# Kernel tuning notes

Measured on AMD Instinct MI355X. Metric: run time of the kernel, lower is better.

## Reference

```python
import jax, jax.numpy as jnp
import numpy as np

PAD = 0  # padding_idx from NlpContext

def setup_inputs() -> dict:
    key = jax.random.key(0)
    k1, k2, k3 = jax.random.split(key, 3)
    B, S, O = 64, 2048, 256
    pred = jax.random.normal(k1, (B, S, O), dtype=jnp.float32)
    gt = jax.random.randint(k2, (B, S), 0, O, dtype=jnp.int64)
    transition = jax.random.normal(k3, (O, O), dtype=jnp.float32)
    return {"pred": pred, "gt": gt, "transition": transition}

def reference(pred, gt, transition):
    B, S, O = pred.shape
    mask = (gt == PAD)
    maskf = mask.astype(pred.dtype)  # (B,S)
    # zero padded positions then log_softmax over labels
    pred = pred * (1.0 - maskf[:, :, None])
    logp = jax.nn.log_softmax(pred, axis=-1)          # (B,S,O)
    trans = jax.nn.log_softmax(transition, axis=-1)   # (O,O)

    # --- hypotheses (path) score ---
    # additive recurrence collapses: alpha = logp[:,0] + sum_t rowsum(logp[:,t]) + T*colsum(trans)
    npl = S - jnp.max(jnp.sum(mask.astype(jnp.int32), axis=1))  # non_pad_length
    tvec = jnp.arange(1, S)
    cond = (npl >= 1) & (npl <= S - 1)  # early-break reachable?
    incl = jnp.where(cond, tvec <= npl, True).astype(pred.dtype)  # (S-1,)
    T = incl.sum()
    row_tot = jnp.sum(logp[:, 1:, :], axis=-1)  # (B,S-1)
    alpha = (logp[:, 0, :]
             + jnp.einsum('bt,t->b', row_tot, incl)[:, None]
             + T * jnp.sum(trans, axis=0)[None, :])  # (B,O)

    # --- gold (null hypothesis) score ---
    emit = jnp.take_along_axis(logp, gt[:, :, None], axis=2)[..., 0]  # (B,S)
    tr_sc = trans[gt[:, :-1], gt[:, 1:]] * (1.0 - maskf[:, 1:])       # (B,S-1)
    gold = jnp.sum(tr_sc + emit[:, 1:] + emit[:, 0:1], axis=1)        # (B,)

    return jnp.mean(alpha - gold[:, None])
```

## Files before the change

### kernel.cpp

```cpp
#include <hip/hip_runtime.h>
#include <math.h>

#define Bn 64
#define Sn 2048
#define On 256
#define PAD 0


__launch_bounds__(256)
__global__ void prep_kernel(const float* __restrict__ trans,
                            const int* __restrict__ gt,
                            float* __restrict__ lse_trans,
                            float* __restrict__ row_total,
                            int* __restrict__ padcnt,
                            double* __restrict__ zreg) {
    int blk = blockIdx.x;
    int tid = threadIdx.x, lane = tid & 63, w = tid >> 6;
    if (blk < On) {
        float x = trans[blk * On + tid];
        float se = __expf(x), sx = x;
        #pragma unroll
        for (int off = 32; off > 0; off >>= 1) {
            se += __shfl_xor(se, off);
            sx += __shfl_xor(sx, off);
        }
        __shared__ float s_se[4], s_sx[4];
        if (lane == 0) { s_se[w] = se; s_sx[w] = sx; }
        __syncthreads();
        if (tid == 0) {
            float SE = (s_se[0] + s_se[1]) + (s_se[2] + s_se[3]);
            float SX = (s_sx[0] + s_sx[1]) + (s_sx[2] + s_sx[3]);
            float lse = __logf(SE);
            lse_trans[blk] = lse;
            row_total[blk] = SX - (float)On * lse;
        }
    } else if (blk < On + Bn) {
        int b = blk - On;
        int cnt = 0;
        for (int i = tid; i < Sn; i += 256) cnt += (gt[b * Sn + i] == PAD) ? 1 : 0;
        #pragma unroll
        for (int off = 32; off > 0; off >>= 1) cnt += __shfl_xor(cnt, off);
        __shared__ int s_c[4];
        if (lane == 0) s_c[w] = cnt;
        __syncthreads();
        if (tid == 0) padcnt[b] = (s_c[0] + s_c[1]) + (s_c[2] + s_c[3]);
    } else {
        int idx = (blk - (On + Bn)) * 256 + tid;
        if (idx < 3072) zreg[idx] = 0.0;
    }
}

__launch_bounds__(256)
__global__ void main_kernel(const float* __restrict__ pred,
                            const int* __restrict__ gt,
                            const float* __restrict__ trans,
                            const float* __restrict__ lse_trans,
                            double* __restrict__ bucket,
                            double* __restrict__ accum) {
    int wave = threadIdx.x >> 6, lane = threadIdx.x & 63;
    int base = blockIdx.x * 16 + wave * 4;
    int b = base >> 11;

    const float4* p4 = reinterpret_cast<const float4*>(pred + (size_t)base * On);
    float4 x0 = p4[lane];
    float4 x1 = p4[64 + lane];
    float4 x2 = p4[128 + lane];
    float4 x3 = p4[192 + lane];

    int li = (lane < 5) ? lane : 4;
    int gi = base - 1 + li; if (gi < 0) gi = 0;
    int gv = gt[gi];
    int g0 = __shfl(gv, 1), g1 = __shfl(gv, 2), g2 = __shfl(gv, 3), g3 = __shfl(gv, 4);
    int q0 = __shfl(gv, 0), q1 = g0, q2 = g1, q3 = g2;

    if (g0 == PAD) { x0.x = 0.f; x0.y = 0.f; x0.z = 0.f; x0.w = 0.f; }
    if (g1 == PAD) { x1.x = 0.f; x1.y = 0.f; x1.z = 0.f; x1.w = 0.f; }
    if (g2 == PAD) { x2.x = 0.f; x2.y = 0.f; x2.z = 0.f; x2.w = 0.f; }
    if (g3 == PAD) { x3.x = 0.f; x3.y = 0.f; x3.z = 0.f; x3.w = 0.f; }

    float se0 = (__expf(x0.x) + __expf(x0.y)) + (__expf(x0.z) + __expf(x0.w));
    float se1 = (__expf(x1.x) + __expf(x1.y)) + (__expf(x1.z) + __expf(x1.w));
    float se2 = (__expf(x2.x) + __expf(x2.y)) + (__expf(x2.z) + __expf(x2.w));
    float se3 = (__expf(x3.x) + __expf(x3.y)) + (__expf(x3.z) + __expf(x3.w));
    float sx0 = (x0.x + x0.y) + (x0.z + x0.w);
    float sx1 = (x1.x + x1.y) + (x1.z + x1.w);
    float sx2 = (x2.x + x2.y) + (x2.z + x2.w);
    float sx3 = (x3.x + x3.y) + (x3.z + x3.w);

    #pragma unroll
    for (int off = 32; off > 0; off >>= 1) {
        se0 += __shfl_xor(se0, off); sx0 += __shfl_xor(sx0, off);
        se1 += __shfl_xor(se1, off); sx1 += __shfl_xor(sx1, off);
        se2 += __shfl_xor(se2, off); sx2 += __shfl_xor(sx2, off);
        se3 += __shfl_xor(se3, off); sx3 += __shfl_xor(sx3, off);
    }
    float lse0 = __logf(se0), lse1 = __logf(se1), lse2 = __logf(se2), lse3 = __logf(se3);
    float rs0 = sx0 - (float)On * lse0;
    float rs1 = sx1 - (float)On * lse1;
    float rs2 = sx2 - (float)On * lse2;
    float rs3 = sx3 - (float)On * lse3;

    int c0 = g0 & 3, c1 = g1 & 3, c2 = g2 & 3, c3 = g3 & 3;
    float xv0 = (c0 == 0) ? x0.x : (c0 == 1) ? x0.y : (c0 == 2) ? x0.z : x0.w;
    float xv1 = (c1 == 0) ? x1.x : (c1 == 1) ? x1.y : (c1 == 2) ? x1.z : x1.w;
    float xv2 = (c2 == 0) ? x2.x : (c2 == 1) ? x2.y : (c2 == 2) ? x2.z : x2.w;
    float xv3 = (c3 == 0) ? x3.x : (c3 == 1) ? x3.y : (c3 == 2) ? x3.z : x3.w;
    float e0 = __shfl(xv0, g0 >> 2) - lse0;
    float e1 = __shfl(xv1, g1 >> 2) - lse1;
    float e2 = __shfl(xv2, g2 >> 2) - lse2;
    float e3 = __shfl(xv3, g3 >> 2) - lse3;

    double goldr = 0.0;
    if (lane < 4) {
        int s = (base + lane) & (Sn - 1);
        int g = (lane == 0) ? g0 : (lane == 1) ? g1 : (lane == 2) ? g2 : g3;
        int q = (lane == 0) ? q0 : (lane == 1) ? q1 : (lane == 2) ? q2 : q3;
        float e  = (lane == 0) ? e0 : (lane == 1) ? e1 : (lane == 2) ? e2 : e3;
        float rs = (lane == 0) ? rs0 : (lane == 1) ? rs1 : (lane == 2) ? rs2 : rs3;
        if (s == 0) {
            goldr = (double)(Sn - 1) * (double)e;
        } else {
            float tr = (g != PAD) ? (trans[q * On + g] - lse_trans[q]) : 0.f;
            goldr = (double)(e + tr);
        }
        unsafeAtomicAdd(&bucket[s], (double)rs);
    }
    goldr += __shfl_xor(goldr, 1);
    goldr += __shfl_xor(goldr, 2);

    __shared__ double gbuf[4];
    if (lane == 0) gbuf[wave] = goldr;
    __syncthreads();
    if (threadIdx.x == 0)
        unsafeAtomicAdd(&accum[b * 16], (gbuf[0] + gbuf[1]) + (gbuf[2] + gbuf[3]));
}

__launch_bounds__(256)
__global__ void final_kernel(const double* __restrict__ bucket,
                             const double* __restrict__ accum,
                             const float* __restrict__ row_total,
                             const int* __restrict__ padcnt,
                             float* __restrict__ out) {
    int tid = threadIdx.x, lane = tid & 63, w = tid >> 6;
    __shared__ int s_npl, s_cond;
    if (tid < 64) {
        int c = padcnt[tid];
        #pragma unroll
        for (int off = 32; off > 0; off >>= 1) c = max(c, __shfl_xor(c, off));
        if (tid == 0) {
            int npl = Sn - c;
            s_npl = npl;
            s_cond = (npl >= 1 && npl <= Sn - 1) ? 1 : 0;
        }
    }
    __syncthreads();
    int npl = s_npl, cond = s_cond;

    double part = 0.0;
    for (int s = tid; s < Sn; s += 256) {
        double wgt = (s == 0) ? (1.0 / On)
                              : (cond ? ((s <= npl) ? 1.0 : 0.0) : 1.0);
        part += wgt * bucket[s];
    }
    if (tid < 64) part -= accum[tid * 16];

    double ttp = (double)row_total[tid];

    #pragma unroll
    for (int off = 32; off > 0; off >>= 1) {
        part += __shfl_xor(part, off);
        ttp  += __shfl_xor(ttp, off);
    }
    __shared__ double rp[4], rt[4];
    if (lane == 0) { rp[w] = part; rt[w] = ttp; }
    __syncthreads();
    if (tid == 0) {
        double hyp_minus_gold = (rp[0] + rp[1]) + (rp[2] + rp[3]);
        double tt = (rt[0] + rt[1]) + (rt[2] + rt[3]);
        int T = cond ? npl : (Sn - 1);
        out[0] = (float)(hyp_minus_gold / (double)Bn + (double)T * tt / (double)On);
    }
}

extern "C" void kernel_launch(void* const* d_in, const int* in_sizes, int n_in,
                              void* d_out, int out_size, void* d_ws, size_t ws_size,
                              hipStream_t stream) {
    const float* pred  = (const float*)d_in[0];
    const int*   gt    = (const int*)d_in[1];
    const float* trans = (const float*)d_in[2];
    float* out = (float*)d_out;

    char* ws = (char*)d_ws;
    double* bucket    = (double*)(ws + 0);
    double* accum     = (double*)(ws + 16384);
    float*  lse_trans = (float*)(ws + 24576);
    float*  row_total = (float*)(ws + 25600);
    int*    padcnt    = (int*)(ws + 26624);

    prep_kernel<<<On + Bn + 16, 256, 0, stream>>>(trans, gt, lse_trans, row_total,
                                                  padcnt, bucket);
    main_kernel<<<(Bn * Sn) / 16, 256, 0, stream>>>(pred, gt, trans, lse_trans,
                                                    bucket, accum);
    final_kernel<<<1, 256, 0, stream>>>(bucket, accum, row_total, padcnt, out);
}
```

Before: 38.77 us.

## Fuse prep and main kernels, drop atomics via per-position blocks and transition histogram

Merges the prep and main kernels into one launch. Each of 2048 blocks owns one sequence position across all 64 batches, so the row-sum and gold partials are written directly instead of accumulated with global double atomics, which also removes the zero-initialisation pass. The lse_trans subtraction is taken out of the per-element gold path: a per-batch histogram of previous labels is built and applied in the final kernel. The cost is strided 1 KB row reads across batches in 1024-thread blocks and an extra histogram reduction in the single-block final kernel.

New measurement: 49.95 us. 28.9% more time.

```diff
diff --git a/kernel.cpp b/kernel.cpp
--- a/kernel.cpp
+++ b/kernel.cpp
@@ -7,139 +7,167 @@
 #define PAD 0
 
 
-__launch_bounds__(256)
-__global__ void prep_kernel(const float* __restrict__ trans,
+__launch_bounds__(1024)
+__global__ void mega_kernel(const float* __restrict__ pred,
                             const int* __restrict__ gt,
+                            const float* __restrict__ trans,
+                            double* __restrict__ bucket,
+                            double* __restrict__ goldraw,
                             float* __restrict__ lse_trans,
                             float* __restrict__ row_total,
                             int* __restrict__ padcnt,
-                            double* __restrict__ zreg) {
+                            int* __restrict__ hist) {
     int blk = blockIdx.x;
-    int tid = threadIdx.x, lane = tid & 63, w = tid >> 6;
-    if (blk < On) {
-        float x = trans[blk * On + tid];
+    int tid = threadIdx.x;
+    int wave = tid >> 6, lane = tid & 63;
+
+    __shared__ double s_bkt[16], s_gld[16];
+    __shared__ float  s_pse[16], s_psx[16];
+    __shared__ int    s_h[256];
+    __shared__ int    s_pc[16];
+
+    if (blk < Sn) {
+        int s = blk;
+        int b0 = wave * 4;
+
+        const float4* r0 = (const float4*)(pred + ((size_t)(b0 + 0) * Sn + s) * On);
+        const float4* r1 = (const float4*)(pred + ((size_t)(b0 + 1) * Sn + s) * On);
+        const float4* r2 = (const float4*)(pred + ((size_t)(b0 + 2) * Sn + s) * On);
+        const float4* r3 = (const float4*)(pred + ((size_t)(b0 + 3) * Sn + s) * On);
+        float4 x0 = r0[lane];
+        float4 x1 = r1[lane];
+        float4 x2 = r2[lane];
+        float4 x3 = r3[lane];
+
+        int gval = 0;
+        if (lane < 8) {
+            int r = lane & 3;
+            long gi = (long)(b0 + r) * Sn + s - ((lane >= 4) ? 1 : 0);
+            if (gi < 0) gi = 0;
+            gval = gt[gi];
+        }
+        int g0 = __shfl(gval, 0), g1 = __shfl(gval, 1);
+        int g2 = __shfl(gval, 2), g3 = __shfl(gval, 3);
+        int q0 = __shfl(gval, 4), q1 = __shfl(gval, 5);
+        int q2 = __shfl(gval, 6), q3 = __shfl(gval, 7);
+
+        if (g0 == PAD) { x0.x = 0.f; x0.y = 0.f; x0.z = 0.f; x0.w = 0.f; }
+        if (g1 == PAD) { x1.x = 0.f; x1.y = 0.f; x1.z = 0.f; x1.w = 0.f; }
+        if (g2 == PAD) { x2.x = 0.f; x2.y = 0.f; x2.z = 0.f; x2.w = 0.f; }
+        if (g3 == PAD) { x3.x = 0.f; x3.y = 0.f; x3.z = 0.f; x3.w = 0.f; }
+
+        float se0 = (__expf(x0.x) + __expf(x0.y)) + (__expf(x0.z) + __expf(x0.w));
+        float se1 = (__expf(x1.x) + __expf(x1.y)) + (__expf(x1.z) + __expf(x1.w));
+        float se2 = (__expf(x2.x) + __expf(x2.y)) + (__expf(x2.z) + __expf(x2.w));
+        float se3 = (__expf(x3.x) + __expf(x3.y)) + (__expf(x3.z) + __expf(x3.w));
+        float sx0 = (x0.x + x0.y) + (x0.z + x0.w);
+        float sx1 = (x1.x + x1.y) + (x1.z + x1.w);
+        float sx2 = (x2.x + x2.y) + (x2.z + x2.w);
+        float sx3 = (x3.x + x3.y) + (x3.z + x3.w);
+
+        #pragma unroll
+        for (int off = 32; off > 0; off >>= 1) {
+            se0 += __shfl_xor(se0, off); sx0 += __shfl_xor(sx0, off);
+            se1 += __shfl_xor(se1, off); sx1 += __shfl_xor(sx1, off);
+            se2 += __shfl_xor(se2, off); sx2 += __shfl_xor(sx2, off);
+            se3 += __shfl_xor(se3, off); sx3 += __shfl_xor(sx3, off);
+        }
+        float lse0 = __logf(se0), lse1 = __logf(se1);
+        float lse2 = __logf(se2), lse3 = __logf(se3);
+        float rs0 = sx0 - (float)On * lse0;
+        float rs1 = sx1 - (float)On * lse1;
+        float rs2 = sx2 - (float)On * lse2;
+        float rs3 = sx3 - (float)On * lse3;
+
+        int c0 = g0 & 3, c1 = g1 & 3, c2 = g2 & 3, c3 = g3 & 3;
+        float xv0 = (c0 == 0) ? x0.x : (c0 == 1) ? x0.y : (c0 == 2) ? x0.z : x0.w;
+        float xv1 = (c1 == 0) ? x1.x : (c1 == 1) ? x1.y : (c1 == 2) ? x1.z : x1.w;
+        float xv2 = (c2 == 0) ? x2.x : (c2 == 1) ? x2.y : (c2 == 2) ? x2.z : x2.w;
+        float xv3 = (c3 == 0) ? x3.x : (c3 == 1) ? x3.y : (c3 == 2) ? x3.z : x3.w;
+        float e0 = __shfl(xv0, g0 >> 2) - lse0;
+        float e1 = __shfl(xv1, g1 >> 2) - lse1;
+        float e2 = __shfl(xv2, g2 >> 2) - lse2;
+        float e3 = __shfl(xv3, g3 >> 2) - lse3;
+
+        if (lane == 0) {
+            double bp = ((double)rs0 + (double)rs1) + ((double)rs2 + (double)rs3);
+            double gp;
+            if (s == 0) {
+                gp = (double)(Sn - 1) *
+                     (((double)e0 + (double)e1) + ((double)e2 + (double)e3));
+            } else {
+                float t0 = (g0 != PAD) ? trans[q0 * On + g0] : 0.f;
+                float t1 = (g1 != PAD) ? trans[q1 * On + g1] : 0.f;
+                float t2 = (g2 != PAD) ? trans[q2 * On + g2] : 0.f;
+                float t3 = (g3 != PAD) ? trans[q3 * On + g3] : 0.f;
+                gp = ((double)(e0 + t0) + (double)(e1 + t1)) +
+                     ((double)(e2 + t2) + (double)(e3 + t3));
+            }
+            s_bkt[wave] = bp;
+            s_gld[wave] = gp;
+        }
+        __syncthreads();
+        if (tid == 0) {
+            double B = 0.0, G = 0.0;
+            #pragma unroll
+            for (int i = 0; i < 16; i++) { B += s_bkt[i]; G += s_gld[i]; }
+            bucket[s] = B;
+            goldraw[s] = G;
+        }
+    } else if (blk < Sn + 64) {
+        int grp = tid >> 8;
+        int col = tid & 255;
+        int i = (blk - Sn) * 4 + grp;
+        float x = trans[i * On + col];
         float se = __expf(x), sx = x;
         #pragma unroll
         for (int off = 32; off > 0; off >>= 1) {
             se += __shfl_xor(se, off);
             sx += __shfl_xor(sx, off);
         }
-        __shared__ float s_se[4], s_sx[4];
-        if (lane == 0) { s_se[w] = se; s_sx[w] = sx; }
+        if (lane == 0) { s_pse[wave] = se; s_psx[wave] = sx; }
+        __syncthreads();
+        if (col == 0) {
+            int w0 = grp * 4;
+            float SE = (s_pse[w0] + s_pse[w0 + 1]) + (s_pse[w0 + 2] + s_pse[w0 + 3]);
+            float SX = (s_psx[w0] + s_psx[w0 + 1]) + (s_psx[w0 + 2] + s_psx[w0 + 3]);
+            float lse = __logf(SE);
+            lse_trans[i] = lse;
+            row_total[i] = SX - (float)On * lse;
+        }
+    } else {
+        int b = blk - (Sn + 64);
+        if (tid < 256) s_h[tid] = 0;
+        __syncthreads();
+        int cnt = 0;
+        for (int s2 = tid; s2 < Sn; s2 += 1024)
+            cnt += (gt[b * Sn + s2] == PAD) ? 1 : 0;
+        for (int s2 = 1 + tid; s2 < Sn; s2 += 1024) {
+            int gcur = gt[b * Sn + s2];
+            int gprev = gt[b * Sn + s2 - 1];
+            if (gcur != PAD) atomicAdd(&s_h[gprev], 1);
+        }
+        #pragma unroll
+        for (int off = 32; off > 0; off >>= 1) cnt += __shfl_xor(cnt, off);
+        if (lane == 0) s_pc[wave] = cnt;
         __syncthreads();
         if (tid == 0) {
-            float SE = (s_se[0] + s_se[1]) + (s_se[2] + s_se[3]);
-            float SX = (s_sx[0] + s_sx[1]) + (s_sx[2] + s_sx[3]);
-            float lse = __logf(SE);
-            lse_trans[blk] = lse;
-            row_total[blk] = SX - (float)On * lse;
-        }
-    } else if (blk < On + Bn) {
-        int b = blk - On;
-        int cnt = 0;
-        for (int i = tid; i < Sn; i += 256) cnt += (gt[b * Sn + i] == PAD) ? 1 : 0;
-        #pragma unroll
-        for (int off = 32; off > 0; off >>= 1) cnt += __shfl_xor(cnt, off);
-        __shared__ int s_c[4];
-        if (lane == 0) s_c[w] = cnt;
-        __syncthreads();
-        if (tid == 0) padcnt[b] = (s_c[0] + s_c[1]) + (s_c[2] + s_c[3]);
-    } else {
-        int idx = (blk - (On + Bn)) * 256 + tid;
-        if (idx < 3072) zreg[idx] = 0.0;
-    }
-}
-
-__launch_bounds__(256)
-__global__ void main_kernel(const float* __restrict__ pred,
-                            const int* __restrict__ gt,
-                            const float* __restrict__ trans,
-                            const float* __restrict__ lse_trans,
-                            double* __restrict__ bucket,
-                            double* __restrict__ accum) {
-    int wave = threadIdx.x >> 6, lane = threadIdx.x & 63;
-    int base = blockIdx.x * 16 + wave * 4;
-    int b = base >> 11;
-
-    const float4* p4 = reinterpret_cast<const float4*>(pred + (size_t)base * On);
-    float4 x0 = p4[lane];
-    float4 x1 = p4[64 + lane];
-    float4 x2 = p4[128 + lane];
-    float4 x3 = p4[192 + lane];
-
-    int li = (lane < 5) ? lane : 4;
-    int gi = base - 1 + li; if (gi < 0) gi = 0;
-    int gv = gt[gi];
-    int g0 = __shfl(gv, 1), g1 = __shfl(gv, 2), g2 = __shfl(gv, 3), g3 = __shfl(gv, 4);
-    int q0 = __shfl(gv, 0), q1 = g0, q2 = g1, q3 = g2;
-
-    if (g0 == PAD) { x0.x = 0.f; x0.y = 0.f; x0.z = 0.f; x0.w = 0.f; }
-    if (g1 == PAD) { x1.x = 0.f; x1.y = 0.f; x1.z = 0.f; x1.w = 0.f; }
-    if (g2 == PAD) { x2.x = 0.f; x2.y = 0.f; x2.z = 0.f; x2.w = 0.f; }
-    if (g3 == PAD) { x3.x = 0.f; x3.y = 0.f; x3.z = 0.f; x3.w = 0.f; }
-
-    float se0 = (__expf(x0.x) + __expf(x0.y)) + (__expf(x0.z) + __expf(x0.w));
-    float se1 = (__expf(x1.x) + __expf(x1.y)) + (__expf(x1.z) + __expf(x1.w));
-    float se2 = (__expf(x2.x) + __expf(x2.y)) + (__expf(x2.z) + __expf(x2.w));
-    float se3 = (__expf(x3.x) + __expf(x3.y)) + (__expf(x3.z) + __expf(x3.w));
-    float sx0 = (x0.x + x0.y) + (x0.z + x0.w);
-    float sx1 = (x1.x + x1.y) + (x1.z + x1.w);
-    float sx2 = (x2.x + x2.y) + (x2.z + x2.w);
-    float sx3 = (x3.x + x3.y) + (x3.z + x3.w);
-
-    #pragma unroll
-    for (int off = 32; off > 0; off >>= 1) {
-        se0 += __shfl_xor(se0, off); sx0 += __shfl_xor(sx0, off);
-        se1 += __shfl_xor(se1, off); sx1 += __shfl_xor(sx1, off);
-        se2 += __shfl_xor(se2, off); sx2 += __shfl_xor(sx2, off);
-        se3 += __shfl_xor(se3, off); sx3 += __shfl_xor(sx3, off);
-    }
-    float lse0 = __logf(se0), lse1 = __logf(se1), lse2 = __logf(se2), lse3 = __logf(se3);
-    float rs0 = sx0 - (float)On * lse0;
-    float rs1 = sx1 - (float)On * lse1;
-    float rs2 = sx2 - (float)On * lse2;
-    float rs3 = sx3 - (float)On * lse3;
-
-    int c0 = g0 & 3, c1 = g1 & 3, c2 = g2 & 3, c3 = g3 & 3;
-    float xv0 = (c0 == 0) ? x0.x : (c0 == 1) ? x0.y : (c0 == 2) ? x0.z : x0.w;
-    float xv1 = (c1 == 0) ? x1.x : (c1 == 1) ? x1.y : (c1 == 2) ? x1.z : x1.w;
-    float xv2 = (c2 == 0) ? x2.x : (c2 == 1) ? x2.y : (c2 == 2) ? x2.z : x2.w;
-    float xv3 = (c3 == 0) ? x3.x : (c3 == 1) ? x3.y : (c3 == 2) ? x3.z : x3.w;
-    float e0 = __shfl(xv0, g0 >> 2) - lse0;
-    float e1 = __shfl(xv1, g1 >> 2) - lse1;
-    float e2 = __shfl(xv2, g2 >> 2) - lse2;
-    float e3 = __shfl(xv3, g3 >> 2) - lse3;
-
-    double goldr = 0.0;
-    if (lane < 4) {
-        int s = (base + lane) & (Sn - 1);
-        int g = (lane == 0) ? g0 : (lane == 1) ? g1 : (lane == 2) ? g2 : g3;
-        int q = (lane == 0) ? q0 : (lane == 1) ? q1 : (lane == 2) ? q2 : q3;
-        float e  = (lane == 0) ? e0 : (lane == 1) ? e1 : (lane == 2) ? e2 : e3;
-        float rs = (lane == 0) ? rs0 : (lane == 1) ? rs1 : (lane == 2) ? rs2 : rs3;
-        if (s == 0) {
-            goldr = (double)(Sn - 1) * (double)e;
-        } else {
-            float tr = (g != PAD) ? (trans[q * On + g] - lse_trans[q]) : 0.f;
-            goldr = (double)(e + tr);
-        }
-        unsafeAtomicAdd(&bucket[s], (double)rs);
-    }
-    goldr += __shfl_xor(goldr, 1);
-    goldr += __shfl_xor(goldr, 2);
-
-    __shared__ double gbuf[4];
-    if (lane == 0) gbuf[wave] = goldr;
-    __syncthreads();
-    if (threadIdx.x == 0)
-        unsafeAtomicAdd(&accum[b * 16], (gbuf[0] + gbuf[1]) + (gbuf[2] + gbuf[3]));
+            int t = 0;
+            #pragma unroll
+            for (int i = 0; i < 16; i++) t += s_pc[i];
+            padcnt[b] = t;
+        }
+        if (tid < 256) hist[b * 256 + tid] = s_h[tid];
+    }
 }
 
 __launch_bounds__(256)
 __global__ void final_kernel(const double* __restrict__ bucket,
-                             const double* __restrict__ accum,
+                             const double* __restrict__ goldraw,
+                             const float* __restrict__ lse_trans,
                              const float* __restrict__ row_total,
                              const int* __restrict__ padcnt,
+                             const int* __restrict__ hist,
                              float* __restrict__ out) {
     int tid = threadIdx.x, lane = tid & 63, w = tid >> 6;
     __shared__ int s_npl, s_cond;
@@ -156,29 +184,34 @@
     __syncthreads();
     int npl = s_npl, cond = s_cond;
 
-    double part = 0.0;
+    double A = 0.0, G = 0.0;
     for (int s = tid; s < Sn; s += 256) {
         double wgt = (s == 0) ? (1.0 / On)
                               : (cond ? ((s <= npl) ? 1.0 : 0.0) : 1.0);
-        part += wgt * bucket[s];
-    }
-    if (tid < 64) part -= accum[tid * 16];
-
-    double ttp = (double)row_total[tid];
+        A += wgt * bucket[s];
+        G += goldraw[s];
+    }
+    int c = 0;
+    for (int b = 0; b < Bn; b++) c += hist[b * 256 + tid];
+    G -= (double)c * (double)lse_trans[tid];
+
+    double tt = (double)row_total[tid];
 
     #pragma unroll
     for (int off = 32; off > 0; off >>= 1) {
-        part += __shfl_xor(part, off);
-        ttp  += __shfl_xor(ttp, off);
-    }
-    __shared__ double rp[4], rt[4];
-    if (lane == 0) { rp[w] = part; rt[w] = ttp; }
+        A  += __shfl_xor(A, off);
+        G  += __shfl_xor(G, off);
+        tt += __shfl_xor(tt, off);
+    }
+    __shared__ double rA[4], rG[4], rT[4];
+    if (lane == 0) { rA[w] = A; rG[w] = G; rT[w] = tt; }
     __syncthreads();
     if (tid == 0) {
-        double hyp_minus_gold = (rp[0] + rp[1]) + (rp[2] + rp[3]);
-        double tt = (rt[0] + rt[1]) + (rt[2] + rt[3]);
+        double At = (rA[0] + rA[1]) + (rA[2] + rA[3]);
+        double Gt = (rG[0] + rG[1]) + (rG[2] + rG[3]);
+        double Tt = (rT[0] + rT[1]) + (rT[2] + rT[3]);
         int T = cond ? npl : (Sn - 1);
-        out[0] = (float)(hyp_minus_gold / (double)Bn + (double)T * tt / (double)On);
+        out[0] = (float)((At - Gt) / (double)Bn + (double)T * Tt / (double)On);
     }
 }
 
@@ -192,14 +225,14 @@
 
     char* ws = (char*)d_ws;
     double* bucket    = (double*)(ws + 0);
-    double* accum     = (double*)(ws + 16384);
-    float*  lse_trans = (float*)(ws + 24576);
-    float*  row_total = (float*)(ws + 25600);
-    int*    padcnt    = (int*)(ws + 26624);
-
-    prep_kernel<<<On + Bn + 16, 256, 0, stream>>>(trans, gt, lse_trans, row_total,
-                                                  padcnt, bucket);
-    main_kernel<<<(Bn * Sn) / 16, 256, 0, stream>>>(pred, gt, trans, lse_trans,
-                                                    bucket, accum);
-    final_kernel<<<1, 256, 0, stream>>>(bucket, accum, row_total, padcnt, out);
+    double* goldraw   = (double*)(ws + 16384);
+    float*  lse_trans = (float*)(ws + 32768);
+    float*  row_total = (float*)(ws + 33792);
+    int*    padcnt    = (int*)(ws + 34816);
+    int*    hist      = (int*)(ws + 35072);
+
+    mega_kernel<<<Sn + 64 + 64, 1024, 0, stream>>>(pred, gt, trans, bucket, goldraw,
+                                                   lse_trans, row_total, padcnt, hist);
+    final_kernel<<<1, 256, 0, stream>>>(bucket, goldraw, lse_trans, row_total,
+                                        padcnt, hist, out);
 }
```

## Replace per-position atomic buckets with per-block partials and in-kernel weighting

Applied to the files above, without the earlier changes.

Each main-kernel block now applies the hypothesis weight (computed from padcnt read inside the block) to its row sums and writes one non-atomic partial per block, instead of making double atomic adds to per-position buckets and per-batch accumulators. The zeroing of the workspace in the prep kernel is dropped, and the final kernel reduces the 8192 partials with 1024 threads. This removes contention from double atomics, but every block now also loads padcnt and does a 64-lane max reduction.

Measured after the change: 38.59 us. About the same (-0.5%).

```diff
diff --git a/kernel.cpp b/kernel.cpp
--- a/kernel.cpp
+++ b/kernel.cpp
@@ -12,8 +12,7 @@
                             const int* __restrict__ gt,
                             float* __restrict__ lse_trans,
                             float* __restrict__ row_total,
-                            int* __restrict__ padcnt,
-                            double* __restrict__ zreg) {
+                            int* __restrict__ padcnt) {
     int blk = blockIdx.x;
     int tid = threadIdx.x, lane = tid & 63, w = tid >> 6;
     if (blk < On) {
@@ -34,7 +33,7 @@
             lse_trans[blk] = lse;
             row_total[blk] = SX - (float)On * lse;
         }
-    } else if (blk < On + Bn) {
+    } else {
         int b = blk - On;
         int cnt = 0;
         for (int i = tid; i < Sn; i += 256) cnt += (gt[b * Sn + i] == PAD) ? 1 : 0;
@@ -44,9 +43,6 @@
         if (lane == 0) s_c[w] = cnt;
         __syncthreads();
         if (tid == 0) padcnt[b] = (s_c[0] + s_c[1]) + (s_c[2] + s_c[3]);
-    } else {
-        int idx = (blk - (On + Bn)) * 256 + tid;
-        if (idx < 3072) zreg[idx] = 0.0;
     }
 }
 
@@ -55,17 +51,22 @@
                             const int* __restrict__ gt,
                             const float* __restrict__ trans,
                             const float* __restrict__ lse_trans,
-                            double* __restrict__ bucket,
-                            double* __restrict__ accum) {
+                            const int* __restrict__ padcnt,
+                            double* __restrict__ partial) {
     int wave = threadIdx.x >> 6, lane = threadIdx.x & 63;
     int base = blockIdx.x * 16 + wave * 4;
-    int b = base >> 11;
 
     const float4* p4 = reinterpret_cast<const float4*>(pred + (size_t)base * On);
     float4 x0 = p4[lane];
     float4 x1 = p4[64 + lane];
     float4 x2 = p4[128 + lane];
     float4 x3 = p4[192 + lane];
+
+    int pc = padcnt[lane];
+    #pragma unroll
+    for (int off = 32; off > 0; off >>= 1) pc = max(pc, __shfl_xor(pc, off));
+    int npl = Sn - pc;
+    int cond = (npl >= 1 && npl <= Sn - 1) ? 1 : 0;
 
     int li = (lane < 5) ? lane : 4;
     int gi = base - 1 + li; if (gi < 0) gi = 0;
@@ -110,7 +111,7 @@
     float e2 = __shfl(xv2, g2 >> 2) - lse2;
     float e3 = __shfl(xv3, g3 >> 2) - lse3;
 
-    double goldr = 0.0;
+    double cval = 0.0;
     if (lane < 4) {
         int s = (base + lane) & (Sn - 1);
         int g = (lane == 0) ? g0 : (lane == 1) ? g1 : (lane == 2) ? g2 : g3;
@@ -118,30 +119,35 @@
         float e  = (lane == 0) ? e0 : (lane == 1) ? e1 : (lane == 2) ? e2 : e3;
         float rs = (lane == 0) ? rs0 : (lane == 1) ? rs1 : (lane == 2) ? rs2 : rs3;
         if (s == 0) {
-            goldr = (double)(Sn - 1) * (double)e;
+            cval = (double)rs * (1.0 / On) - (double)(Sn - 1) * (double)e;
         } else {
+            float wgt = cond ? ((s <= npl) ? 1.0f : 0.0f) : 1.0f;
             float tr = (g != PAD) ? (trans[q * On + g] - lse_trans[q]) : 0.f;
-            goldr = (double)(e + tr);
+            cval = (double)wgt * (double)rs - (double)(e + tr);
         }
-        unsafeAtomicAdd(&bucket[s], (double)rs);
     }
-    goldr += __shfl_xor(goldr, 1);
-    goldr += __shfl_xor(goldr, 2);
+    cval += __shfl_xor(cval, 1);
+    cval += __shfl_xor(cval, 2);
 
-    __shared__ double gbuf[4];
-    if (lane == 0) gbuf[wave] = goldr;
+    __shared__ double cbuf[4];
+    if (lane == 0) cbuf[wave] = cval;
     __syncthreads();
     if (threadIdx.x == 0)
-        unsafeAtomicAdd(&accum[b * 16], (gbuf[0] + gbuf[1]) + (gbuf[2] + gbuf[3]));
+        partial[blockIdx.x] = (cbuf[0] + cbuf[1]) + (cbuf[2] + cbuf[3]);
 }
 
-__launch_bounds__(256)
-__global__ void final_kernel(const double* __restrict__ bucket,
-                             const double* __restrict__ accum,
+__launch_bounds__(1024)
+__global__ void final_kernel(const double* __restrict__ partial,
                              const float* __restrict__ row_total,
                              const int* __restrict__ padcnt,
                              float* __restrict__ out) {
     int tid = threadIdx.x, lane = tid & 63, w = tid >> 6;
+
+    double P = 0.0;
+    #pragma unroll
+    for (int i = 0; i < 8; i++) P += partial[tid + i * 1024];
+    double tt = (tid < On) ? (double)row_total[tid] : 0.0;
+
     __shared__ int s_npl, s_cond;
     if (tid < 64) {
         int c = padcnt[tid];
@@ -153,32 +159,22 @@
             s_cond = (npl >= 1 && npl <= Sn - 1) ? 1 : 0;
         }
     }
-    __syncthreads();
-    int npl = s_npl, cond = s_cond;
-
-    double part = 0.0;
-    for (int s = tid; s < Sn; s += 256) {
-        double wgt = (s == 0) ? (1.0 / On)
-                              : (cond ? ((s <= npl) ? 1.0 : 0.0) : 1.0);
-        part += wgt * bucket[s];
-    }
-    if (tid < 64) part -= accum[tid * 16];
-
-    double ttp = (double)row_total[tid];
 
     #pragma unroll
     for (int off = 32; off > 0; off >>= 1) {
-        part += __shfl_xor(part, off);
-        ttp  += __shfl_xor(ttp, off);
+        P  += __shfl_xor(P, off);
+        tt += __shfl_xor(tt, off);
     }
-    __shared__ double rp[4], rt[4];
-    if (lane == 0) { rp[w] = part; rt[w] = ttp; }
+    __shared__ double rP[16], rT[16];
+    if (lane == 0) { rP[w] = P; rT[w] = tt; }
     __syncthreads();
     if (tid == 0) {
-        double hyp_minus_gold = (rp[0] + rp[1]) + (rp[2] + rp[3]);
-        double tt = (rt[0] + rt[1]) + (rt[2] + rt[3]);
+        double Pt = 0.0, Tt = 0.0;
+        #pragma unroll
+        for (int i = 0; i < 16; i++) { Pt += rP[i]; Tt += rT[i]; }
+        int npl = s_npl, cond = s_cond;
         int T = cond ? npl : (Sn - 1);
-        out[0] = (float)(hyp_minus_gold / (double)Bn + (double)T * tt / (double)On);
+        out[0] = (float)(Pt / (double)Bn + (double)T * Tt / (double)On);
     }
 }
 
@@ -191,15 +187,13 @@
     float* out = (float*)d_out;
 
     char* ws = (char*)d_ws;
-    double* bucket    = (double*)(ws + 0);
-    double* accum     = (double*)(ws + 16384);
-    float*  lse_trans = (float*)(ws + 24576);
-    float*  row_total = (float*)(ws + 25600);
-    int*    padcnt    = (int*)(ws + 26624);
+    double* partial   = (double*)(ws + 0);
+    float*  lse_trans = (float*)(ws + 65536);
+    float*  row_total = (float*)(ws + 66560);
+    int*    padcnt    = (int*)(ws + 67584);
 
-    prep_kernel<<<On + Bn + 16, 256, 0, stream>>>(trans, gt, lse_trans, row_total,
-                                                  padcnt, bucket);
+    prep_kernel<<<On + Bn, 256, 0, stream>>>(trans, gt, lse_trans, row_total, padcnt);
     main_kernel<<<(Bn * Sn) / 16, 256, 0, stream>>>(pred, gt, trans, lse_trans,
-                                                    bucket, accum);
-    final_kernel<<<1, 256, 0, stream>>>(bucket, accum, row_total, padcnt, out);
+                                                    padcnt, partial);
+    final_kernel<<<1, 1024, 0, stream>>>(partial, row_total, padcnt, out);
 }
```
